# Performance work log

Measured on AMD Instinct MI355X. Metric: run time of the kernel, lower is better.

## Reference

```python
import jax, jax.numpy as jnp
import numpy as np

N_EMBD = 2048
N_HEAD = 16
D_HEAD = N_EMBD // N_HEAD  # 128
B, T = 2, 2048
ROPE_BASE = 10000.0


def _rope_cos_sin(T, d, dtype):
    # (T, d) cos/sin tables, rotate-half convention
    inv_freq = 1.0 / (ROPE_BASE ** (jnp.arange(0, d, 2, dtype=jnp.float32) / d))
    ang = jnp.arange(T, dtype=jnp.float32)[:, None] * inv_freq[None, :]  # (T, d/2)
    cos = jnp.concatenate([jnp.cos(ang), jnp.cos(ang)], axis=-1).astype(dtype)
    sin = jnp.concatenate([jnp.sin(ang), jnp.sin(ang)], axis=-1).astype(dtype)
    return cos, sin


def _rotate_half(x):
    d = x.shape[-1] // 2
    return jnp.concatenate([-x[..., d:], x[..., :d]], axis=-1)


def setup_inputs() -> dict:
    key = jax.random.key(0)
    k1, k2, k3 = jax.random.split(key, 3)
    x = jax.random.normal(k1, (B, T, N_EMBD), dtype=jnp.float32)
    w_qkv = jax.random.normal(k2, (3 * N_EMBD, N_EMBD), dtype=jnp.float32) * 0.02
    w_proj = jax.random.normal(k3, (N_EMBD, N_EMBD), dtype=jnp.float32) * 0.02
    return {"x": x, "w_qkv": w_qkv, "w_proj": w_proj}


def reference(x, w_qkv, w_proj):
    Bq, Tq, C = x.shape
    H, D = N_HEAD, D_HEAD
    # fused QKV projection (torch Linear: x @ W.T)
    qkv = jnp.einsum('btc,fc->btf', x, w_qkv).reshape(Bq, Tq, 3, H, D)
    q, k, v = qkv[:, :, 0], qkv[:, :, 1], qkv[:, :, 2]  # (B,T,H,D)
    q = jnp.transpose(q, (0, 2, 1, 3))  # (B,H,T,D)
    k = jnp.transpose(k, (0, 2, 1, 3))
    v = jnp.transpose(v, (0, 2, 1, 3))
    # RoPE (start_pos = 0)
    cos, sin = _rope_cos_sin(Tq, D, x.dtype)  # (T,D)
    q = q * cos[None, None] + _rotate_half(q) * sin[None, None]
    k = k * cos[None, None] + _rotate_half(k) * sin[None, None]
    # causal SDPA
    scale = 1.0 / jnp.sqrt(jnp.asarray(D, x.dtype))
    scores = jnp.einsum('bhqd,bhkd->bhqk', q, k) * scale  # (B,H,T,T)
    causal = jnp.tril(jnp.ones((Tq, Tq), dtype=bool))
    scores = jnp.where(causal[None, None], scores, jnp.asarray(-jnp.inf, x.dtype))
    attn = jax.nn.softmax(scores, axis=-1)
    y = jnp.einsum('bhqk,bhkd->bhqd', attn, v)  # (B,H,T,D)
    y = jnp.transpose(y, (0, 2, 1, 3)).reshape(Bq, Tq, C)
    y = jnp.einsum('btc,fc->btf', y, w_proj)
    return y
```

## Files before the change

### kernel.cpp

```cpp
#include <hip/hip_runtime.h>
#include <hip/hip_bf16.h>
#include <math.h>

typedef __attribute__((ext_vector_type(8))) short short8;
typedef __attribute__((ext_vector_type(4))) short short4_t;
typedef __attribute__((ext_vector_type(4))) float f32x4;

#define Bb 2
#define Tt 2048
#define Hh 16
#define Dd 128
#define Cc 2048
#define Ff 6144

__device__ __forceinline__ size_t packed_idx(int row, int k) {
  return ((((size_t)(row >> 7) * 64 + (k >> 5)) * 8 + ((row >> 4) & 7)) * 512)
         + ((((k >> 3) & 3) * 16 + (row & 15)) * 8) + (k & 7);
}

__device__ __forceinline__ void gload_lds16(const void* g, void* l) {
  __builtin_amdgcn_global_load_lds(
      (const __attribute__((address_space(1))) void*)g,
      (__attribute__((address_space(3))) void*)l, 16, 0, 0);
}

__global__ __launch_bounds__(256) void pack_cast(
    const float* __restrict__ in, __hip_bfloat16* __restrict__ out, int n16)
{
  int t = blockIdx.x * 256 + threadIdx.x;
  if (t >= n16) return;
  int l = t & 63;
  int granule_lin = t >> 6;
  int g = granule_lin & 7;
  int slab = granule_lin >> 3;
  int ks = slab & 63;
  int m_tile = slab >> 6;
  int row = m_tile * 128 + g * 16 + (l & 15);
  int k = ks * 32 + (l >> 4) * 8;
  const float* src = in + (size_t)row * 2048 + k;
  float4 v0 = *(const float4*)src;
  float4 v1 = *(const float4*)(src + 4);
  __hip_bfloat16 tmp[8] = {
      __float2bfloat16(v0.x), __float2bfloat16(v0.y),
      __float2bfloat16(v0.z), __float2bfloat16(v0.w),
      __float2bfloat16(v1.x), __float2bfloat16(v1.y),
      __float2bfloat16(v1.z), __float2bfloat16(v1.w)};
  *(short8*)(out + (size_t)t * 8) = *(const short8*)tmp;
}

__device__ __forceinline__ void store_out(__hip_bfloat16* p, float v) { *p = __float2bfloat16(v); }
__device__ __forceinline__ void store_out(float* p, float v) { *p = v; }

template <typename OutT>
__global__ __launch_bounds__(256) void gemm_pk(
    const __hip_bfloat16* __restrict__ Ap,
    const __hip_bfloat16* __restrict__ Bp,
    OutT* __restrict__ Cm,
    int K, int N)
{
  __shared__ __align__(16) __hip_bfloat16 As[128 * 32];
  __shared__ __align__(16) __hip_bfloat16 Bs[128 * 32];
  const int tid  = threadIdx.x;
  const int wave = tid >> 6;
  const int lane = tid & 63;
  const int quad = lane >> 4;
  const int l16  = lane & 15;
  const int bm = blockIdx.y * 128;
  const int bn = blockIdx.x * 128;
  const int wm4 = (wave >> 1) * 4;
  const int wn4 = (wave & 1) * 4;
  const int KS = K >> 5;

  f32x4 acc[4][4];
#pragma unroll
  for (int i = 0; i < 4; i++)
#pragma unroll
    for (int j = 0; j < 4; j++)
#pragma unroll
      for (int r = 0; r < 4; r++) acc[i][j][r] = 0.f;

  const char* pA[2];
  const char* pB[2];
#pragma unroll
  for (int c = 0; c < 2; c++) {
    int g = wave * 2 + c;
    pA[c] = (const char*)Ap + (size_t)(bm >> 7) * KS * 8192 + g * 1024 + lane * 16;
    pB[c] = (const char*)Bp + (size_t)(bn >> 7) * KS * 8192 + g * 1024 + lane * 16;
  }

  for (int ks = 0; ks < KS; ks++) {
#pragma unroll
    for (int c = 0; c < 2; c++) {
      int g = wave * 2 + c;
      gload_lds16(pA[c], As + g * 512);
      gload_lds16(pB[c], Bs + g * 512);
      pA[c] += 8192;
      pB[c] += 8192;
    }
    __syncthreads();
    short8 af[4], bf[4];
#pragma unroll
    for (int i = 0; i < 4; i++)
      af[i] = *(const short8*)(As + (wm4 + i) * 512 + lane * 8);
#pragma unroll
    for (int j = 0; j < 4; j++)
      bf[j] = *(const short8*)(Bs + (wn4 + j) * 512 + lane * 8);
#pragma unroll
    for (int i = 0; i < 4; i++)
#pragma unroll
      for (int j = 0; j < 4; j++)
        acc[i][j] = __builtin_amdgcn_mfma_f32_16x16x32_bf16(af[i], bf[j], acc[i][j], 0, 0, 0);
    __syncthreads();
  }

#pragma unroll
  for (int i = 0; i < 4; i++)
#pragma unroll
    for (int j = 0; j < 4; j++)
#pragma unroll
      for (int r = 0; r < 4; r++) {
        int gm = bm + (wave >> 1) * 64 + i * 16 + quad * 4 + r;
        int gn = bn + (wave & 1) * 64 + j * 16 + l16;
        store_out(Cm + (size_t)gm * N + gn, acc[i][j][r]);
      }
}

__global__ __launch_bounds__(256) void rope_qk(__hip_bfloat16* __restrict__ qkv)
{
  int tid = blockIdx.x * 256 + threadIdx.x;
  int d = tid & 63;
  int h = (tid >> 6) & 15;
  int t = (tid >> 10) & 2047;
  int bw = tid >> 21;
  int b = bw & 1, which = bw >> 1;
  size_t base = (size_t)(b * Tt + t) * Ff + which * 2048 + h * Dd + d;
  float inv = expf(-(float)d * (9.210340371976184f / 64.0f));
  float ang = (float)t * inv;
  float c = cosf(ang), s = sinf(ang);
  float x1 = __bfloat162float(qkv[base]);
  float x2 = __bfloat162float(qkv[base + 64]);
  float o1 = x1 * c - x2 * s;
  float o2 = x2 * c + x1 * s;
  if (which == 0) {
    o1 *= 0.08838834764831845f;
    o2 *= 0.08838834764831845f;
  }
  qkv[base]      = __float2bfloat16(o1);
  qkv[base + 64] = __float2bfloat16(o2);
}

__global__ __launch_bounds__(256) void transpose_v(
    const __hip_bfloat16* __restrict__ qkv, __hip_bfloat16* __restrict__ vt)
{
  __shared__ __hip_bfloat16 tile[64 * 65];
  int bh = blockIdx.y;
  int dt = blockIdx.x >> 5;
  int tt = blockIdx.x & 31;
  int b = bh >> 4, h = bh & 15;
  const __hip_bfloat16* src = qkv + (size_t)(b * Tt + tt * 64) * Ff + 4096 + h * Dd + dt * 64;
#pragma unroll
  for (int i = 0; i < 16; i++) {
    int lin = i * 256 + threadIdx.x;
    int tl = lin >> 6, dc = lin & 63;
    tile[tl * 65 + dc] = src[(size_t)tl * Ff + dc];
  }
  __syncthreads();
  __hip_bfloat16* dst = vt + ((size_t)bh * Dd + dt * 64) * Tt + tt * 64;
#pragma unroll
  for (int i = 0; i < 16; i++) {
    int lin = i * 256 + threadIdx.x;
    int dr = lin >> 6, tc = lin & 63;
    dst[(size_t)dr * Tt + tc] = tile[tc * 65 + dr];
  }
}

__global__ __launch_bounds__(512) void flash_attn3(
    const __hip_bfloat16* __restrict__ qkv,
    const __hip_bfloat16* __restrict__ vt,
    __hip_bfloat16* __restrict__ yat)
{
  __shared__ __align__(16) __hip_bfloat16 KsBuf[2][8192];
  __shared__ __align__(16) __hip_bfloat16 VsBuf[8192];
  __shared__ __align__(16) __hip_bfloat16 PsBuf[8 * 1088];
  const int tid  = threadIdx.x;
  const int wave = tid >> 6;
  const int lane = tid & 63;
  const int quad = lane >> 4;
  const int l16  = lane & 15;
  const int idx  = blockIdx.x;
  const int top  = idx >> 8;
  const int rest = idx & 255;
  const int p    = rest >> 5;
  const int bh   = rest & 31;
  const int qi   = top ? (15 - p) : p;
  const int b = bh >> 4, h = bh & 15;

  const char* kbase = (const char*)(qkv + (size_t)b * Tt * Ff + 2048 + h * Dd);
  const char* vbase = (const char*)(vt + (size_t)bh * Dd * Tt);
  __hip_bfloat16* Pw = PsBuf + wave * 1088;
  const int srow = lane & 15;
  const int scol = lane >> 4;

  const int qm0 = qi * 128;
  const int niter = 2 * qi + 2;

  short8 qf[4];
  {
    const __hip_bfloat16* qrow =
        qkv + (size_t)(b * Tt + qm0 + wave * 16 + l16) * Ff + h * Dd;
#pragma unroll
    for (int kc = 0; kc < 4; kc++)
      qf[kc] = *(const short8*)(qrow + kc * 32 + quad * 8);
  }

#pragma unroll
  for (int c = 0; c < 2; c++) {
    int chunk = wave * 2 + c;
    int j = chunk >> 2, kc = chunk & 3;
    const char* src = kbase + (size_t)(j * 16 + srow) * (Ff * 2) + kc * 64 + scol * 16;
    gload_lds16(src, KsBuf[0] + chunk * 512);
  }

  f32x4 oacc[8];
#pragma unroll
  for (int jd = 0; jd < 8; jd++)
#pragma unroll
    for (int r = 0; r < 4; r++) oacc[jd][r] = 0.f;
  float mrow[4], lrow[4];
#pragma unroll
  for (int r = 0; r < 4; r++) { mrow[r] = -INFINITY; lrow[r] = 0.f; }

#pragma unroll 1
  for (int kt = 0; kt < niter; ++kt) {
    __builtin_amdgcn_s_barrier();
#pragma unroll
    for (int c = 0; c < 2; c++) {
      int chunk = wave * 2 + c;
      int jd = chunk >> 1, k2 = chunk & 1;
      const char* src = vbase + (size_t)(jd * 16 + srow) * (Tt * 2) + kt * 128 + k2 * 64 + scol * 16;
      gload_lds16(src, VsBuf + chunk * 512);
    }
    if (kt + 1 < niter) {
#pragma unroll
      for (int c = 0; c < 2; c++) {
        int chunk = wave * 2 + c;
        int j = chunk >> 2, kc = chunk & 3;
        const char* src = kbase + (size_t)((kt + 1) * 64 + j * 16 + srow) * (Ff * 2) + kc * 64 + scol * 16;
        gload_lds16(src, KsBuf[(kt + 1) & 1] + chunk * 512);
      }
      __builtin_amdgcn_s_waitcnt(0xF74);
    } else {
      __builtin_amdgcn_s_waitcnt(0xF72);
    }
    __builtin_amdgcn_s_barrier();

    const __hip_bfloat16* KsB = KsBuf[kt & 1];
    const bool diag = (kt >= 2 * qi);

    f32x4 sacc[4];
#pragma unroll
    for (int j = 0; j < 4; j++)
#pragma unroll
      for (int r = 0; r < 4; r++) sacc[j][r] = 0.f;
#pragma unroll
    for (int j = 0; j < 4; j++)
#pragma unroll
      for (int kc = 0; kc < 4; kc++) {
        short8 kf = *(const short8*)(KsB + (j * 4 + kc) * 512 + lane * 8);
        sacc[j] = __builtin_amdgcn_mfma_f32_16x16x32_bf16(qf[kc], kf, sacc[j], 0, 0, 0);
      }
    float sv[4][4];
#pragma unroll
    for (int j = 0; j < 4; j++)
#pragma unroll
      for (int r = 0; r < 4; r++) {
        float v = sacc[j][r];
        if (diag) {
          int kg = kt * 64 + j * 16 + l16;
          int qg = qm0 + wave * 16 + quad * 4 + r;
          if (kg > qg) v = -INFINITY;
        }
        sv[j][r] = v;
      }
    float mnew[4];
#pragma unroll
    for (int r = 0; r < 4; r++)
      mnew[r] = fmaxf(fmaxf(sv[0][r], sv[1][r]), fmaxf(sv[2][r], sv[3][r]));
#pragma unroll
    for (int off = 1; off < 16; off <<= 1)
#pragma unroll
      for (int r = 0; r < 4; r++)
        mnew[r] = fmaxf(mnew[r], __shfl_xor(mnew[r], off, 64));
    float alpha[4];
#pragma unroll
    for (int r = 0; r < 4; r++) {
      float mi = fmaxf(mrow[r], mnew[r]);
      alpha[r] = __expf(mrow[r] - mi);
      mrow[r] = mi;
    }
    float rs[4] = {0.f, 0.f, 0.f, 0.f};
#pragma unroll
    for (int j = 0; j < 4; j++)
#pragma unroll
      for (int r = 0; r < 4; r++) {
        float p2 = __expf(sv[j][r] - mrow[r]);
        rs[r] += p2;
        Pw[(j * 2 + (l16 >> 3)) * 136 + (quad * 4 + r) * 8 + (l16 & 7)] = __float2bfloat16(p2);
      }
#pragma unroll
    for (int off = 1; off < 16; off <<= 1)
#pragma unroll
      for (int r = 0; r < 4; r++)
        rs[r] += __shfl_xor(rs[r], off, 64);
#pragma unroll
    for (int r = 0; r < 4; r++) lrow[r] = lrow[r] * alpha[r] + rs[r];
#pragma unroll
    for (int jd = 0; jd < 8; jd++)
#pragma unroll
      for (int r = 0; r < 4; r++) oacc[jd][r] *= alpha[r];

    if (kt + 1 < niter) {
      __builtin_amdgcn_s_waitcnt(0xF72);
    } else {
      __builtin_amdgcn_s_waitcnt(0xF70);
    }
    __builtin_amdgcn_s_barrier();

#pragma unroll
    for (int k2 = 0; k2 < 2; k2++) {
      short8 pf = *(const short8*)(Pw + (k2 * 4 + quad) * 136 + l16 * 8);
#pragma unroll
      for (int jd = 0; jd < 8; jd++) {
        short8 vf = *(const short8*)(VsBuf + (jd * 2 + k2) * 512 + lane * 8);
        oacc[jd] = __builtin_amdgcn_mfma_f32_16x16x32_bf16(pf, vf, oacc[jd], 0, 0, 0);
      }
    }
  }

  float linv[4];
#pragma unroll
  for (int r = 0; r < 4; r++) linv[r] = 1.f / lrow[r];
#pragma unroll
  for (int jd = 0; jd < 8; jd++)
#pragma unroll
    for (int r = 0; r < 4; r++) {
      int row = b * Tt + qm0 + wave * 16 + quad * 4 + r;
      int c = h * Dd + jd * 16 + l16;
      yat[packed_idx(row, c)] = __float2bfloat16(oacc[jd][r] * linv[r]);
    }
}

extern "C" void kernel_launch(void* const* d_in, const int* in_sizes, int n_in,
                              void* d_out, int out_size, void* d_ws, size_t ws_size,
                              hipStream_t stream) {
  (void)in_sizes; (void)n_in; (void)out_size; (void)ws_size;
  const float* x_f      = (const float*)d_in[0];
  const float* w_qkv_f  = (const float*)d_in[1];
  const float* w_proj_f = (const float*)d_in[2];
  float* out = (float*)d_out;

  char* ws = (char*)d_ws;
  __hip_bfloat16* qkv = (__hip_bfloat16*)ws;
  __hip_bfloat16* vt  = (__hip_bfloat16*)(ws + 50331648);
  __hip_bfloat16* yat = (__hip_bfloat16*)(ws + 67108864);
  __hip_bfloat16* xb  = (__hip_bfloat16*)(ws + 83886080);
  __hip_bfloat16* wqb = (__hip_bfloat16*)(ws + 100663296);
  __hip_bfloat16* wpb = (__hip_bfloat16*)(ws + 125829120);

  pack_cast<<<4096, 256, 0, stream>>>(x_f, xb, 1048576);
  pack_cast<<<6144, 256, 0, stream>>>(w_qkv_f, wqb, 1572864);
  pack_cast<<<2048, 256, 0, stream>>>(w_proj_f, wpb, 524288);

  gemm_pk<__hip_bfloat16><<<dim3(48, 32), 256, 0, stream>>>(xb, wqb, qkv, 2048, 6144);
  rope_qk<<<32768, 256, 0, stream>>>(qkv);
  transpose_v<<<dim3(64, 32), 256, 0, stream>>>(qkv, vt);
  flash_attn3<<<512, 512, 0, stream>>>(qkv, vt, yat);
  gemm_pk<float><<<dim3(16, 32), 256, 0, stream>>>(yat, wpb, out, 2048, 2048);
}
```

Baseline: 448.0 us.

## Add 256x256 eight-wave QKV GEMM with double-buffered LDS and phased prefetch

Replaces the QKV projection GEMM with a new kernel that uses 256x256 output tiles, 8 waves per block, and a double-buffered LDS staging scheme. Global-to-LDS loads for the next K-tile are split into four chunks, each issued between MFMA phases, and s_setprio raises priority around the MFMA bursts. The larger tile increases data reuse per LDS load, and the interleaving is meant to hide load latency. In exchange it uses 128KB of LDS and a large accumulator register footprint, which limits occupancy, and it leaves only 384 blocks to fill the GPU.

New measurement: 437.6 us. 1.02x faster.

```diff
diff --git a/kernel.cpp b/kernel.cpp
--- a/kernel.cpp
+++ b/kernel.cpp
@@ -125,6 +125,161 @@
       }
 }
 
+#define GEMM8_PHASE(MB)                                                        \
+  {                                                                            \
+    short8 af[2][2];                                                           \
+    _Pragma("unroll") for (int i = 0; i < 2; i++)                              \
+      _Pragma("unroll") for (int k2 = 0; k2 < 2; k2++)                         \
+        af[i][k2] = *(const short8*)(Ard + (k2 * 8 + MB + i) * 512 + lane * 8);\
+    __builtin_amdgcn_s_barrier();                                              \
+    __builtin_amdgcn_s_setprio(1);                                             \
+    _Pragma("unroll") for (int i = 0; i < 2; i++)                              \
+      _Pragma("unroll") for (int j = 0; j < 4; j++)                            \
+        _Pragma("unroll") for (int k2 = 0; k2 < 2; k2++)                       \
+          acc[MB + i][j] = __builtin_amdgcn_mfma_f32_16x16x32_bf16(            \
+              af[i][k2], bf[j][k2], acc[MB + i][j], 0, 0, 0);                  \
+    __builtin_amdgcn_s_setprio(0);                                             \
+    __builtin_amdgcn_s_barrier();                                              \
+  }
+
+__global__ __launch_bounds__(512, 2) void gemm_pk8(
+    const __hip_bfloat16* __restrict__ Ap,
+    const __hip_bfloat16* __restrict__ Bp,
+    __hip_bfloat16* __restrict__ Cm, int N)
+{
+  __shared__ __align__(16) __hip_bfloat16 L[65536];
+  const int tid  = threadIdx.x;
+  const int wave = tid >> 6;
+  const int lane = tid & 63;
+  const int quad = lane >> 4;
+  const int l16  = lane & 15;
+  const int wm = wave >> 2;
+  const int wn = wave & 3;
+  const int bm = blockIdx.y * 256;
+  const int bn = blockIdx.x * 256;
+  const int NT = 32;
+  const int gl = wave * 2;
+  const int rb = (wn & 1) * 4;
+
+  const char* pA[2][2];
+  const char* pB[2][2];
+#pragma unroll
+  for (int hh = 0; hh < 2; hh++)
+#pragma unroll
+    for (int c = 0; c < 2; c++) {
+      int g = gl + c;
+      pA[hh][c] = (const char*)Ap +
+          (size_t)(((bm >> 7) + hh) * 64 + (g >> 3)) * 8192 + (g & 7) * 1024 + lane * 16;
+      pB[hh][c] = (const char*)Bp +
+          (size_t)(((bn >> 7) + hh) * 64 + (g >> 3)) * 8192 + (g & 7) * 1024 + lane * 16;
+    }
+
+#pragma unroll
+  for (int hh = 0; hh < 2; hh++) {
+#pragma unroll
+    for (int c = 0; c < 2; c++)
+      gload_lds16(pA[hh][c], &L[hh * 16384 + (gl + c) * 512]);
+#pragma unroll
+    for (int c = 0; c < 2; c++)
+      gload_lds16(pB[hh][c], &L[hh * 16384 + 8192 + (gl + c) * 512]);
+  }
+#pragma unroll
+  for (int hh = 0; hh < 2; hh++)
+#pragma unroll
+    for (int c = 0; c < 2; c++) { pA[hh][c] += 16384; pB[hh][c] += 16384; }
+
+  f32x4 acc[8][4];
+#pragma unroll
+  for (int i = 0; i < 8; i++)
+#pragma unroll
+    for (int j = 0; j < 4; j++)
+#pragma unroll
+      for (int r = 0; r < 4; r++) acc[i][j][r] = 0.f;
+
+#pragma unroll 1
+  for (int t = 0; t < NT; ++t) {
+    const int tp = t & 1;
+    const __hip_bfloat16* Ard = &L[(wm + 2 * tp) * 16384];
+    const __hip_bfloat16* Brd = &L[((wn >> 1) + 2 * tp) * 16384 + 8192];
+    __hip_bfloat16* wrA0 = &L[(2 - 2 * tp) * 16384];
+    __hip_bfloat16* wrB0 = wrA0 + 8192;
+    __hip_bfloat16* wrA1 = wrA0 + 16384;
+    __hip_bfloat16* wrB1 = wrA1 + 8192;
+    const bool pre = (t + 1 < NT);
+
+    if (pre) {
+      gload_lds16(pA[0][0], wrA0 + (gl + 0) * 512);
+      gload_lds16(pA[0][1], wrA0 + (gl + 1) * 512);
+      __builtin_amdgcn_s_waitcnt(0xF72);
+    } else {
+      __builtin_amdgcn_s_waitcnt(0xF70);
+    }
+    __builtin_amdgcn_s_barrier();
+
+    short8 bf[4][2];
+#pragma unroll
+    for (int j = 0; j < 4; j++)
+#pragma unroll
+      for (int k2 = 0; k2 < 2; k2++)
+        bf[j][k2] = *(const short8*)(Brd + (k2 * 8 + rb + j) * 512 + lane * 8);
+    {
+      short8 af[2][2];
+#pragma unroll
+      for (int i = 0; i < 2; i++)
+#pragma unroll
+        for (int k2 = 0; k2 < 2; k2++)
+          af[i][k2] = *(const short8*)(Ard + (k2 * 8 + i) * 512 + lane * 8);
+      __builtin_amdgcn_s_setprio(1);
+#pragma unroll
+      for (int i = 0; i < 2; i++)
+#pragma unroll
+        for (int j = 0; j < 4; j++)
+#pragma unroll
+          for (int k2 = 0; k2 < 2; k2++)
+            acc[i][j] = __builtin_amdgcn_mfma_f32_16x16x32_bf16(
+                af[i][k2], bf[j][k2], acc[i][j], 0, 0, 0);
+      __builtin_amdgcn_s_setprio(0);
+    }
+    __builtin_amdgcn_s_barrier();
+
+    if (pre) {
+      gload_lds16(pB[0][0], wrB0 + (gl + 0) * 512);
+      gload_lds16(pB[0][1], wrB0 + (gl + 1) * 512);
+    }
+    GEMM8_PHASE(2);
+
+    if (pre) {
+      gload_lds16(pA[1][0], wrA1 + (gl + 0) * 512);
+      gload_lds16(pA[1][1], wrA1 + (gl + 1) * 512);
+    }
+    GEMM8_PHASE(4);
+
+    if (pre) {
+      gload_lds16(pB[1][0], wrB1 + (gl + 0) * 512);
+      gload_lds16(pB[1][1], wrB1 + (gl + 1) * 512);
+    }
+    GEMM8_PHASE(6);
+
+    if (pre) {
+#pragma unroll
+      for (int hh = 0; hh < 2; hh++)
+#pragma unroll
+        for (int c = 0; c < 2; c++) { pA[hh][c] += 16384; pB[hh][c] += 16384; }
+    }
+  }
+
+#pragma unroll
+  for (int i = 0; i < 8; i++)
+#pragma unroll
+    for (int j = 0; j < 4; j++)
+#pragma unroll
+      for (int r = 0; r < 4; r++) {
+        int gm = bm + wm * 128 + i * 16 + quad * 4 + r;
+        int gn = bn + wn * 64 + j * 16 + l16;
+        Cm[(size_t)gm * N + gn] = __float2bfloat16(acc[i][j][r]);
+      }
+}
+
 __global__ __launch_bounds__(256) void rope_qk(__hip_bfloat16* __restrict__ qkv)
 {
   int tid = blockIdx.x * 256 + threadIdx.x;
@@ -371,7 +526,7 @@
   pack_cast<<<6144, 256, 0, stream>>>(w_qkv_f, wqb, 1572864);
   pack_cast<<<2048, 256, 0, stream>>>(w_proj_f, wpb, 524288);
 
-  gemm_pk<__hip_bfloat16><<<dim3(48, 32), 256, 0, stream>>>(xb, wqb, qkv, 2048, 6144);
+  gemm_pk8<<<dim3(24, 16), 512, 0, stream>>>(xb, wqb, qkv, 6144);
   rope_qk<<<32768, 256, 0, stream>>>(qkv);
   transpose_v<<<dim3(64, 32), 256, 0, stream>>>(qkv, vt);
   flash_attn3<<<512, 512, 0, stream>>>(qkv, vt, yat);
```
